# Kernel optimization log

Hardware: AMD Instinct MI355X
Metric: run time of the kernel (lower is better)

The kernel has to match this reference:

```python
import jax, jax.numpy as jnp
import numpy as np
import math

# ---- dims ----
B, N, IN_DIM = 4, 512, 128
D, H, DH = 256, 8, 32          # embed_dim, heads, dim_head
L = 8                           # performer depth
M = int(DH * math.log(DH))      # 110 FAVOR+ random features (performer_pytorch default)
HID = 256                       # lstm hidden
FF = 4 * D
EPS_K = 1e-4                    # kernel feature eps
EPS_D = 1e-6                    # denominator eps


def setup_inputs() -> dict:
    key = jax.random.key(0)
    ks = iter(jax.random.split(key, 40))
    def nrm(shape, s=0.02):
        return jax.random.normal(next(ks), shape, dtype=jnp.float32) * s
    z = lambda shape: jnp.zeros(shape, jnp.float32)
    o = lambda shape: jnp.ones(shape, jnp.float32)
    return {
        "x": jax.random.normal(next(ks), (B, N, IN_DIM), dtype=jnp.float32),
        # input projection
        "Win_w": nrm((D, IN_DIM)), "Win_b": z((D,)),
        # performer layers (stacked over L)
        "ln1_w": o((L, D)), "ln1_b": z((L, D)),
        "Wq": nrm((L, D, D)), "bq": z((L, D)),
        "Wk": nrm((L, D, D)), "bk": z((L, D)),
        "Wv": nrm((L, D, D)), "bv": z((L, D)),
        "Wo": nrm((L, D, D)), "bo": z((L, D)),
        "proj": jax.random.normal(next(ks), (L, M, DH), dtype=jnp.float32),  # FAVOR+ projections
        "ln2_w": o((L, D)), "ln2_b": z((L, D)),
        "Wff1": nrm((L, FF, D)), "bff1": z((L, FF)),
        "Wff2": nrm((L, D, FF)), "bff2": z((L, D)),
        # BiLSTM: layer0 input D, layers1-2 input 2*HID; [dir] / [layer,dir] stacks
        "Wih0": nrm((2, 4 * HID, D)), "Whh0": nrm((2, 4 * HID, HID)), "b0": z((2, 2, 4 * HID)),
        "Wih12": nrm((2, 2, 4 * HID, 2 * HID)), "Whh12": nrm((2, 2, 4 * HID, HID)), "b12": z((2, 2, 2, 4 * HID)),
        # final head
        "fc_w": nrm((1, 2 * HID)), "fc_b": z((1,)),
    }


def layer_norm(x, w, b):
    mu = jnp.mean(x, -1, keepdims=True)
    var = jnp.mean((x - mu) ** 2, -1, keepdims=True)
    return (x - mu) * jax.lax.rsqrt(var + 1e-5) * w + b


def softmax_features(x, proj, is_query):
    # FAVOR+ positive softmax-kernel features. x:[b,h,n,dh], proj:[m,dh]
    xd = x * (DH ** -0.25)
    dd = jnp.einsum('bhnd,md->bhnm', xd, proj)
    diag = 0.5 * jnp.sum(xd * xd, -1)[..., None]            # [b,h,n,1]
    if is_query:
        stab = jnp.max(dd, axis=-1, keepdims=True)
    else:
        stab = jnp.max(dd, axis=(-2, -1), keepdims=True)
    return (M ** -0.5) * (jnp.exp(dd - diag - stab) + EPS_K)


def causal_linear_attention(qp, kp, v):
    # qp,kp:[b,h,n,m], v:[b,h,n,dv] -> [b,h,n,dv]; cumulative-sum causal form
    k_cum = jnp.cumsum(kp, axis=2)
    d_inv = 1.0 / (jnp.einsum('bhnm,bhnm->bhn', qp, k_cum) + EPS_D)
    ctx = jnp.cumsum(jnp.einsum('bhnm,bhnd->bhnmd', kp, v), axis=2)
    return jnp.einsum('bhnmd,bhnm,bhn->bhnd', ctx, qp, d_inv)


def performer_block(x, p):
    (lw1, lb1, wq, bq_, wk, bk_, wv, bv_, wo, bo_, pr, lw2, lb2, w1, b1, w2, b2) = p
    b, n = x.shape[0], x.shape[1]
    y = layer_norm(x, lw1, lb1)
    sh = lambda t: t.reshape(b, n, H, DH).transpose(0, 2, 1, 3)
    q = sh(y @ wq.T + bq_)
    k = sh(y @ wk.T + bk_)
    v = sh(y @ wv.T + bv_)
    qp = softmax_features(q, pr, True)
    kp = softmax_features(k, pr, False)
    o = causal_linear_attention(qp, kp, v)
    o = o.transpose(0, 2, 1, 3).reshape(b, n, D)
    x = x + o @ wo.T + bo_
    y = layer_norm(x, lw2, lb2)
    x = x + jax.nn.gelu(y @ w1.T + b1, approximate=False) @ w2.T + b2
    return x, None


def lstm_dir(x, wih, whh, b, reverse):
    # x:[B,N,in] -> hs:[B,N,HID]; torch gate order i,f,g,o
    xs = jnp.flip(x, 1) if reverse else x
    gi = xs.transpose(1, 0, 2) @ wih.T + b                  # [N,B,4H] precomputed input part
    def step(carry, g_in):
        h, c = carry
        g = g_in + h @ whh.T
        i, f, gg, oo = jnp.split(g, 4, axis=-1)
        c = jax.nn.sigmoid(f) * c + jax.nn.sigmoid(i) * jnp.tanh(gg)
        h = jax.nn.sigmoid(oo) * jnp.tanh(c)
        return (h, c), h
    h0 = jnp.zeros((x.shape[0], HID), x.dtype)
    _, hs = jax.lax.scan(step, (h0, h0), gi)
    hs = hs.transpose(1, 0, 2)
    return jnp.flip(hs, 1) if reverse else hs


def bilstm_layer(x, wih, whh, b):
    fwd = lstm_dir(x, wih[0], whh[0], b[0, 0] + b[0, 1], False)
    bwd = lstm_dir(x, wih[1], whh[1], b[1, 0] + b[1, 1], True)
    return jnp.concatenate([fwd, bwd], -1)


def reference(x, Win_w, Win_b, ln1_w, ln1_b, Wq, bq, Wk, bk, Wv, bv, Wo, bo, proj,
              ln2_w, ln2_b, Wff1, bff1, Wff2, bff2,
              Wih0, Whh0, b0, Wih12, Whh12, b12, fc_w, fc_b):
    h = x @ Win_w.T + Win_b
    params = (ln1_w, ln1_b, Wq, bq, Wk, bk, Wv, bv, Wo, bo, proj, ln2_w, ln2_b, Wff1, bff1, Wff2, bff2)
    h, _ = jax.lax.scan(performer_block, h, params)       # 8 performer layers
    # dropout is identity at eval
    h = bilstm_layer(h, Wih0, Whh0, b0)
    h = bilstm_layer(h, Wih12[0], Whh12[0], b12[0])
    h = bilstm_layer(h, Wih12[1], Whh12[1], b12[1])
    return h[:, -1, :] @ fc_w.T + fc_b                    # [B,1]
```

## Files before the change

### kernel.cpp

```cpp
#include <hip/hip_runtime.h>
#include <math.h>

#define B_    4
#define N_    512
#define D_    256
#define H_    8
#define DH_   32
#define M_    110
#define MP_   112
#define FF_   1024
#define HID_  256
#define ROWS_ 2048
#define CHUNK 32
#define NCH   16

#define OFF_H      0u
#define OFF_Y      524288u
#define OFF_Q      1048576u
#define OFF_K      1572864u
#define OFF_V      2097152u
#define OFF_O      2621440u
#define OFF_FF     3145728u
#define OFF_QP     5242880u
#define OFF_KP     7077888u
#define OFF_S      8912896u
#define OFF_MB     9437184u
#define OFF_P      10747904u
#define OFF_KSUM   12582912u
#define OFF_PK     12640256u
#define OFF_DIAG   12697600u
#define OFF_KMAX   12713984u

#define SCALE_X 0.42044820762685725f
#define SCALE_M 0.09534625892455924f

__device__ __forceinline__ float sigmoidf_(float x){ return 1.0f/(1.0f+expf(-x)); }
__device__ __forceinline__ float geluf_(float x){ return 0.5f*x*(1.0f+erff(x*0.70710678118654752f)); }
__device__ __forceinline__ unsigned encf_(float x){ unsigned u=__float_as_uint(x); return (u&0x80000000u)?~u:(u|0x80000000u); }
__device__ __forceinline__ float decf_(unsigned u){ return (u&0x80000000u)?__uint_as_float(u&0x7fffffffu):__uint_as_float(~u); }

typedef unsigned u32x4_ __attribute__((ext_vector_type(4)));
typedef float    f32x4_ __attribute__((ext_vector_type(4)));

__device__ __forceinline__ u32x4_ ld4_l2_(const unsigned* p){
  u32x4_ v;
  asm volatile("global_load_dwordx4 %0, %1, off sc0\n\ts_waitcnt vmcnt(0)"
               : "=v"(v) : "v"(p));
  return v;
}
__device__ __forceinline__ u32x4_ ld4_far_(const unsigned* p){
  u32x4_ v;
  asm volatile("global_load_dwordx4 %0, %1, off sc0 sc1\n\ts_waitcnt vmcnt(0)"
               : "=v"(v) : "v"(p));
  return v;
}
__device__ __forceinline__ void st_l2_(float* p, float x){
  asm volatile("global_store_dword %0, %1, off sc0" :: "v"(p), "v"(x) : "memory");
}
__device__ __forceinline__ f32x4_ ld4_pin_(const float* p){
  f32x4_ v;
  asm volatile("global_load_dwordx4 %0, %1, off\n\ts_waitcnt vmcnt(0)"
               : "=v"(v) : "v"(p));
  return v;
}

__global__ __launch_bounds__(256) void gemm_k(
    const float* __restrict__ A, const float* __restrict__ W,
    const float* __restrict__ b1, const float* __restrict__ b2,
    const float* __restrict__ R, float* __restrict__ C,
    int M, int N, int K, int act)
{
  __shared__ float As[16][72];
  __shared__ float Ws[16][72];
  const int tid = threadIdx.x;
  const int tx = tid & 15, ty = tid >> 4;
  const int i0 = blockIdx.y * 64, j0 = blockIdx.x * 64;
  const int lr = tid >> 2, lc = (tid & 3) << 2;
  float acc[4][4] = {};
  for (int k0 = 0; k0 < K; k0 += 16) {
    float4 a4 = *(const float4*)(A + (size_t)(i0 + lr) * K + k0 + lc);
    float4 w4 = *(const float4*)(W + (size_t)(j0 + lr) * K + k0 + lc);
    __syncthreads();
    As[lc+0][lr]=a4.x; As[lc+1][lr]=a4.y; As[lc+2][lr]=a4.z; As[lc+3][lr]=a4.w;
    Ws[lc+0][lr]=w4.x; Ws[lc+1][lr]=w4.y; Ws[lc+2][lr]=w4.z; Ws[lc+3][lr]=w4.w;
    __syncthreads();
    #pragma unroll
    for (int kk = 0; kk < 16; kk++) {
      float4 av = *(const float4*)&As[kk][ty*4];
      float4 wv = *(const float4*)&Ws[kk][tx*4];
      acc[0][0] += av.x*wv.x; acc[0][1] += av.x*wv.y; acc[0][2] += av.x*wv.z; acc[0][3] += av.x*wv.w;
      acc[1][0] += av.y*wv.x; acc[1][1] += av.y*wv.y; acc[1][2] += av.y*wv.z; acc[1][3] += av.y*wv.w;
      acc[2][0] += av.z*wv.x; acc[2][1] += av.z*wv.y; acc[2][2] += av.z*wv.z; acc[2][3] += av.z*wv.w;
      acc[3][0] += av.w*wv.x; acc[3][1] += av.w*wv.y; acc[3][2] += av.w*wv.z; acc[3][3] += av.w*wv.w;
    }
  }
  #pragma unroll
  for (int ii = 0; ii < 4; ii++) {
    int gi_ = i0 + ty*4 + ii;
    #pragma unroll
    for (int jj = 0; jj < 4; jj++) {
      int gj = j0 + tx*4 + jj;
      float v = acc[ii][jj];
      if (b1) v += b1[gj];
      if (b2) v += b2[gj];
      if (act) v = geluf_(v);
      if (R) v += R[(size_t)gi_ * N + gj];
      C[(size_t)gi_ * N + gj] = v;
    }
  }
}

__global__ __launch_bounds__(256) void gemm3_k(
    const float* __restrict__ A,
    const float* __restrict__ W0, const float* __restrict__ W1, const float* __restrict__ W2,
    const float* __restrict__ c0_, const float* __restrict__ c1_, const float* __restrict__ c2_,
    float* __restrict__ O0, float* __restrict__ O1, float* __restrict__ O2)
{
  const int which = blockIdx.x >> 2;
  const float* W  = which == 0 ? W0 : which == 1 ? W1 : W2;
  const float* bb = which == 0 ? c0_ : which == 1 ? c1_ : c2_;
  float* C        = which == 0 ? O0 : which == 1 ? O1 : O2;
  __shared__ float As[16][72];
  __shared__ float Ws[16][72];
  const int tid = threadIdx.x;
  const int tx = tid & 15, ty = tid >> 4;
  const int i0 = blockIdx.y * 64, j0 = (blockIdx.x & 3) * 64;
  const int lr = tid >> 2, lc = (tid & 3) << 2;
  float acc[4][4] = {};
  for (int k0 = 0; k0 < 256; k0 += 16) {
    float4 a4 = *(const float4*)(A + (size_t)(i0 + lr) * 256 + k0 + lc);
    float4 w4 = *(const float4*)(W + (size_t)(j0 + lr) * 256 + k0 + lc);
    __syncthreads();
    As[lc+0][lr]=a4.x; As[lc+1][lr]=a4.y; As[lc+2][lr]=a4.z; As[lc+3][lr]=a4.w;
    Ws[lc+0][lr]=w4.x; Ws[lc+1][lr]=w4.y; Ws[lc+2][lr]=w4.z; Ws[lc+3][lr]=w4.w;
    __syncthreads();
    #pragma unroll
    for (int kk = 0; kk < 16; kk++) {
      float4 av = *(const float4*)&As[kk][ty*4];
      float4 wv = *(const float4*)&Ws[kk][tx*4];
      acc[0][0] += av.x*wv.x; acc[0][1] += av.x*wv.y; acc[0][2] += av.x*wv.z; acc[0][3] += av.x*wv.w;
      acc[1][0] += av.y*wv.x; acc[1][1] += av.y*wv.y; acc[1][2] += av.y*wv.z; acc[1][3] += av.y*wv.w;
      acc[2][0] += av.z*wv.x; acc[2][1] += av.z*wv.y; acc[2][2] += av.z*wv.z; acc[2][3] += av.z*wv.w;
      acc[3][0] += av.w*wv.x; acc[3][1] += av.w*wv.y; acc[3][2] += av.w*wv.z; acc[3][3] += av.w*wv.w;
    }
  }
  #pragma unroll
  for (int ii = 0; ii < 4; ii++) {
    int gi_ = i0 + ty*4 + ii;
    #pragma unroll
    for (int jj = 0; jj < 4; jj++) {
      int gj = j0 + tx*4 + jj;
      C[(size_t)gi_ * 256 + gj] = acc[ii][jj] + bb[gj];
    }
  }
}

__global__ __launch_bounds__(256) void gemmgi_k(
    const float* __restrict__ A, const float* __restrict__ W, const float* __restrict__ bvec,
    float* __restrict__ C, int K, int wGap, int bGap)
{
  const int dir = blockIdx.x >> 4;
  const float* Wd = W + (size_t)dir * wGap;
  const float* b1 = bvec + (size_t)dir * bGap;
  const float* b2 = b1 + 1024;
  float* Cd = C + (size_t)dir * 2097152;
  __shared__ float As[16][72];
  __shared__ float Ws[16][72];
  const int tid = threadIdx.x;
  const int tx = tid & 15, ty = tid >> 4;
  const int i0 = blockIdx.y * 64, j0 = (blockIdx.x & 15) * 64;
  const int lr = tid >> 2, lc = (tid & 3) << 2;
  float acc[4][4] = {};
  for (int k0 = 0; k0 < K; k0 += 16) {
    float4 a4 = *(const float4*)(A + (size_t)(i0 + lr) * K + k0 + lc);
    float4 w4 = *(const float4*)(Wd + (size_t)(j0 + lr) * K + k0 + lc);
    __syncthreads();
    As[lc+0][lr]=a4.x; As[lc+1][lr]=a4.y; As[lc+2][lr]=a4.z; As[lc+3][lr]=a4.w;
    Ws[lc+0][lr]=w4.x; Ws[lc+1][lr]=w4.y; Ws[lc+2][lr]=w4.z; Ws[lc+3][lr]=w4.w;
    __syncthreads();
    #pragma unroll
    for (int kk = 0; kk < 16; kk++) {
      float4 av = *(const float4*)&As[kk][ty*4];
      float4 wv = *(const float4*)&Ws[kk][tx*4];
      acc[0][0] += av.x*wv.x; acc[0][1] += av.x*wv.y; acc[0][2] += av.x*wv.z; acc[0][3] += av.x*wv.w;
      acc[1][0] += av.y*wv.x; acc[1][1] += av.y*wv.y; acc[1][2] += av.y*wv.z; acc[1][3] += av.y*wv.w;
      acc[2][0] += av.z*wv.x; acc[2][1] += av.z*wv.y; acc[2][2] += av.z*wv.z; acc[2][3] += av.z*wv.w;
      acc[3][0] += av.w*wv.x; acc[3][1] += av.w*wv.y; acc[3][2] += av.w*wv.z; acc[3][3] += av.w*wv.w;
    }
  }
  #pragma unroll
  for (int ii = 0; ii < 4; ii++) {
    int gi_ = i0 + ty*4 + ii;
    #pragma unroll
    for (int jj = 0; jj < 4; jj++) {
      int gj = j0 + tx*4 + jj;
      Cd[(size_t)gi_ * 1024 + gj] = acc[ii][jj] + b1[gj] + b2[gj];
    }
  }
}

__global__ __launch_bounds__(256) void ln_k(const float* __restrict__ x, const float* __restrict__ w,
                                            const float* __restrict__ b, float* __restrict__ y)
{
  const int row = blockIdx.x, t = threadIdx.x;
  float v = x[(size_t)row * 256 + t];
  float s = v;
  #pragma unroll
  for (int o = 32; o >= 1; o >>= 1) s += __shfl_xor(s, o, 64);
  __shared__ float w1_[4], w2_[4];
  const int wid = t >> 6, lane = t & 63;
  if (lane == 0) w1_[wid] = s;
  __syncthreads();
  float mu = (w1_[0] + w1_[1] + w1_[2] + w1_[3]) * (1.0f/256.0f);
  float d = v - mu;
  float s2 = d * d;
  #pragma unroll
  for (int o = 32; o >= 1; o >>= 1) s2 += __shfl_xor(s2, o, 64);
  if (lane == 0) w2_[wid] = s2;
  __syncthreads();
  float var = (w2_[0] + w2_[1] + w2_[2] + w2_[3]) * (1.0f/256.0f);
  y[(size_t)row * 256 + t] = d * (1.0f / sqrtf(var + 1e-5f)) * w[t] + b[t];
}

__global__ __launch_bounds__(256) void feat_k(const float* __restrict__ q, const float* __restrict__ kk,
                                              const float* __restrict__ proj,
                                              float* __restrict__ qp, float* __restrict__ kpraw,
                                              float* __restrict__ diagb, unsigned* __restrict__ kmax)
{
  const int isq = (blockIdx.x < 4096);
  const int bx = isq ? blockIdx.x : (blockIdx.x - 4096);
  const int wid = threadIdx.x >> 6, lane = threadIdx.x & 63;
  const int p = bx * 4 + wid;
  const int bh = p >> 9, n = p & 511;
  const int b = bh >> 3, h = bh & 7;
  __shared__ float xs[4][32];
  const float* xrow = (isq ? q : kk) + ((size_t)(b * N_ + n)) * D_ + h * DH_;
  if (lane < 32) xs[wid][lane] = xrow[lane] * SCALE_X;
  __syncthreads();
  float diag = 0.f;
  #pragma unroll
  for (int d = 0; d < 32; d++) { float xv = xs[wid][d]; diag += xv * xv; }
  diag *= 0.5f;
  const int m0 = lane, m1 = 64 + lane;
  float dd0 = 0.f, dd1 = -INFINITY;
  #pragma unroll
  for (int d = 0; d < 32; d++) dd0 += xs[wid][d] * proj[m0 * 32 + d];
  if (m1 < M_) {
    float a = 0.f;
    #pragma unroll
    for (int d = 0; d < 32; d++) a += xs[wid][d] * proj[m1 * 32 + d];
    dd1 = a;
  }
  float mx = fmaxf(dd0, dd1);
  #pragma unroll
  for (int o = 32; o >= 1; o >>= 1) mx = fmaxf(mx, __shfl_xor(mx, o, 64));
  if (isq) {
    float* out = qp + (size_t)p * MP_;
    out[m0] = SCALE_M * (expf(dd0 - diag - mx) + 1e-4f);
    if (m1 < M_)        out[m1] = SCALE_M * (expf(dd1 - diag - mx) + 1e-4f);
    else if (m1 < MP_)  out[m1] = 0.f;
  } else {
    float* out = kpraw + (size_t)p * MP_;
    out[m0] = dd0;
    if (m1 < M_) out[m1] = dd1;
    if (lane == 0) { diagb[p] = diag; atomicMax(kmax + bh, encf_(mx)); }
  }
}

__global__ __launch_bounds__(256) void csum_k(const float* __restrict__ kp, const float* __restrict__ v,
                                              const float* __restrict__ diagb, const unsigned* __restrict__ kmax,
                                              float* __restrict__ S, float* __restrict__ ksum)
{
  const int bh = blockIdx.x >> 4, c = blockIdx.x & 15;
  const int b = bh >> 3, h = bh & 7;
  __shared__ float kpc[CHUNK * MP_];
  __shared__ float vc[CHUNK][DH_];
  const float* kpbase = kp + ((size_t)bh * N_ + c * CHUNK) * MP_;
  const float kmx = decf_(kmax[bh]);
  const int r0 = bh * N_ + c * CHUNK;
  for (int f = threadIdx.x; f < CHUNK * MP_; f += 256) {
    int i = f / MP_, m = f - i * MP_;
    float raw = kpbase[f];
    float val = 0.f;
    if (m < M_) val = SCALE_M * (expf(raw - diagb[r0 + i] - kmx) + 1e-4f);
    kpc[f] = val;
  }
  for (int f = threadIdx.x; f < CHUNK * DH_; f += 256) {
    int i = f >> 5, d = f & 31;
    vc[i][d] = v[((size_t)(b * N_ + c * CHUNK + i)) * D_ + h * DH_ + d];
  }
  __syncthreads();
  const int d = threadIdx.x & 31, mg = threadIdx.x >> 5;
  float Sa[14] = {};
  for (int i = 0; i < CHUNK; i++) {
    float vv = vc[i][d];
    #pragma unroll
    for (int j = 0; j < 14; j++) Sa[j] += kpc[i * MP_ + mg * 14 + j] * vv;
  }
  float* Sout = S + (((size_t)blockIdx.x) * MP_ + mg * 14) * DH_ + d;
  #pragma unroll
  for (int j = 0; j < 14; j++) Sout[(size_t)j * DH_] = Sa[j];
  if (threadIdx.x < MP_) {
    float s = 0.f;
    for (int i = 0; i < CHUNK; i++) s += kpc[i * MP_ + threadIdx.x];
    ksum[(size_t)blockIdx.x * MP_ + threadIdx.x] = s;
  }
}

__global__ __launch_bounds__(256) void cpref_k(const float* __restrict__ S, const float* __restrict__ ksum,
                                               float* __restrict__ P, float* __restrict__ pk)
{
  const int bh = blockIdx.x;
  const int d = threadIdx.x & 31, mg = threadIdx.x >> 5;
  float run[14] = {};
  for (int c = 0; c < NCH; c++) {
    size_t base = (((size_t)(bh * NCH + c)) * MP_ + mg * 14) * DH_ + d;
    #pragma unroll
    for (int j = 0; j < 14; j++) { P[base + (size_t)j * DH_] = run[j]; run[j] += S[base + (size_t)j * DH_]; }
  }
  if (threadIdx.x < MP_) {
    float r = 0.f;
    for (int c = 0; c < NCH; c++) {
      size_t o = (size_t)(bh * NCH + c) * MP_ + threadIdx.x;
      pk[o] = r; r += ksum[o];
    }
  }
}

__global__ __launch_bounds__(256, 1) void attn_k(const float* __restrict__ qp, const float* __restrict__ kp,
                                                 const float* __restrict__ v, const float* __restrict__ P,
                                                 const float* __restrict__ pk,
                                                 const float* __restrict__ diagb, const unsigned* __restrict__ kmax,
                                                 float* __restrict__ o)
{
  const int bh = blockIdx.x >> 4, c = blockIdx.x & 15;
  const int b = bh >> 3, h = bh & 7;
  __shared__ float qpc[CHUNK * 113];
  __shared__ float kpc[CHUNK * 113];
  __shared__ float vc[CHUNK][DH_];
  __shared__ float Pl[MP_ * DH_];
  __shared__ float pkl[MP_];
  __shared__ float Al[CHUNK * 33];
  __shared__ float den[CHUNK];
  const int t = threadIdx.x;
  const float* qbase = qp + ((size_t)bh * N_ + c * CHUNK) * MP_;
  const float* kbase = kp + ((size_t)bh * N_ + c * CHUNK) * MP_;
  const float kmx = decf_(kmax[bh]);
  const int r0 = bh * N_ + c * CHUNK;
  for (int f = t; f < CHUNK * MP_; f += 256) {
    int i = f / MP_, m = f - i * MP_;
    qpc[i * 113 + m] = qbase[f];
    float raw = kbase[f];
    float val = 0.f;
    if (m < M_) val = SCALE_M * (expf(raw - diagb[r0 + i] - kmx) + 1e-4f);
    kpc[i * 113 + m] = val;
  }
  for (int f = t; f < CHUNK * DH_; f += 256) {
    int i = f >> 5, d = f & 31;
    vc[i][d] = v[((size_t)(b * N_ + c * CHUNK + i)) * D_ + h * DH_ + d];
  }
  for (int f = t; f < MP_ * DH_; f += 256) Pl[f] = P[((size_t)blockIdx.x) * MP_ * DH_ + f];
  if (t < MP_) pkl[t] = pk[(size_t)blockIdx.x * MP_ + t];
  __syncthreads();
  {
    const int ti = t >> 4, tj = t & 15;
    float a00 = 0.f, a01 = 0.f, a10 = 0.f, a11 = 0.f;
    for (int m = 0; m < MP_; m++) {
      float q0 = qpc[(ti*2+0)*113 + m], q1 = qpc[(ti*2+1)*113 + m];
      float k0 = kpc[(tj*2+0)*113 + m], k1 = kpc[(tj*2+1)*113 + m];
      a00 += q0*k0; a01 += q0*k1; a10 += q1*k0; a11 += q1*k1;
    }
    const int i0_ = ti*2, j0_ = tj*2;
    Al[(i0_  )*33 + j0_  ] = (j0_   <= i0_  ) ? a00 : 0.f;
    Al[(i0_  )*33 + j0_+1] = (j0_+1 <= i0_  ) ? a01 : 0.f;
    Al[(i0_+1)*33 + j0_  ] = (j0_   <= i0_+1) ? a10 : 0.f;
    Al[(i0_+1)*33 + j0_+1] = (j0_+1 <= i0_+1) ? a11 : 0.f;
  }
  __syncthreads();
  if (t < CHUNK) {
    const int i = t; float s = 0.f;
    for (int m = 0; m < MP_; m++) s += qpc[i*113 + m] * pkl[m];
    for (int j = 0; j <= i; j++) s += Al[i*33 + j];
    den[i] = 1.0f / (s + 1e-6f);
  }
  __syncthreads();
  {
    const int d = t & 31, ig = t >> 5;
    float Pd[MP_];
    #pragma unroll
    for (int m = 0; m < MP_; m++) Pd[m] = Pl[m * DH_ + d];
    float vd[CHUNK];
    #pragma unroll
    for (int j = 0; j < CHUNK; j++) vd[j] = vc[j][d];
    for (int r = 0; r < 4; r++) {
      const int i = ig * 4 + r;
      float acc = 0.f;
      #pragma unroll
      for (int m = 0; m < MP_; m++) acc += qpc[i*113 + m] * Pd[m];
      #pragma unroll
      for (int j = 0; j < CHUNK; j++) acc += Al[i*33 + j] * vd[j];
      o[((size_t)(b * N_ + c * CHUNK + i)) * D_ + h * DH_ + d] = acc * den[i];
    }
  }
}

__global__ __launch_bounds__(256, 1) void rec_k(
    const float* __restrict__ gi, const float* __restrict__ whh,
    float* __restrict__ hs, float* __restrict__ hxa, float* __restrict__ hxb)
{
  const int bid = blockIdx.x;
  if ((bid & 7) > 1) return;
  const int dir = bid & 7;
  const int s = bid >> 3;
  if (s >= 16) return;
  const int t = threadIdx.x;

  const float* giD = gi + (size_t)dir * 2097152;
  const float* whD = whh + (size_t)dir * 262144;
  float* hxaD = hxa + (size_t)dir * 524288;
  float* hxbD = hxb + (size_t)dir * 524288;

  __shared__ __align__(16) float h_sh[4][256];
  __shared__ __align__(16) float red[64 * 33];

  __builtin_amdgcn_fence(__ATOMIC_ACQUIRE, "agent");

  const int rg = t & 31, kq = t >> 5;
  f32x4_ w4[2][8];
  #pragma unroll
  for (int rr = 0; rr < 2; rr++) {
    const int rho = rg * 2 + rr;
    const int grow = (rho >> 4) * 256 + s * 16 + (rho & 15);
    const float* src = whD + (size_t)grow * 256 + kq * 32;
    #pragma unroll
    for (int q = 0; q < 8; q++) w4[rr][q] = ld4_pin_(src + q * 4);
  }

  const int j = t & 15, bb = t >> 4;
  const float* pgi0 = giD + (size_t)bb * 524288 + (size_t)(s * 16 + j);

  ((float4*)h_sh)[t] = make_float4(0.f, 0.f, 0.f, 0.f);
  float c0 = 0.f;
  __syncthreads();

  int n = dir ? 511 : 0;
  float gnext[4];
  if (t < 64) {
    #pragma unroll
    for (int g = 0; g < 4; g++) gnext[g] = pgi0[(size_t)n * 1024 + g * 256];
  }

  for (int step = 0; step < 512; step++) {
    const int n2 = dir ? (510 - step) : (step + 1);
    float gcur[4];
    if (t < 64) {
      #pragma unroll
      for (int g = 0; g < 4; g++) gcur[g] = gnext[g];
      if (step < 511) {
        #pragma unroll
        for (int g = 0; g < 4; g++) gnext[g] = pgi0[(size_t)n2 * 1024 + g * 256];
      }
    }

    float acc[2][4] = {};
    #pragma unroll
    for (int q = 0; q < 8; q++) {
      f32x4_ h0 = *(const f32x4_*)&h_sh[0][kq * 32 + q * 4];
      f32x4_ h1 = *(const f32x4_*)&h_sh[1][kq * 32 + q * 4];
      f32x4_ h2 = *(const f32x4_*)&h_sh[2][kq * 32 + q * 4];
      f32x4_ h3 = *(const f32x4_*)&h_sh[3][kq * 32 + q * 4];
      #pragma unroll
      for (int rr = 0; rr < 2; rr++) {
        f32x4_ w = w4[rr][q];
        acc[rr][0] += w.x*h0.x + w.y*h0.y + w.z*h0.z + w.w*h0.w;
        acc[rr][1] += w.x*h1.x + w.y*h1.y + w.z*h1.z + w.w*h1.w;
        acc[rr][2] += w.x*h2.x + w.y*h2.y + w.z*h2.z + w.w*h2.w;
        acc[rr][3] += w.x*h3.x + w.y*h3.y + w.z*h3.z + w.w*h3.w;
      }
    }
    #pragma unroll
    for (int rr = 0; rr < 2; rr++)
      #pragma unroll
      for (int b = 0; b < 4; b++)
        red[(rg * 2 + rr) * 33 + b * 8 + kq] = acc[rr][b];
    __syncthreads();

    if (t < 64) {
      float pre[4];
      #pragma unroll
      for (int g = 0; g < 4; g++) {
        const float* rp = &red[(g * 16 + j) * 33 + bb * 8];
        float sum = gcur[g];
        #pragma unroll
        for (int q = 0; q < 8; q++) sum += rp[q];
        pre[g] = sum;
      }
      c0 = sigmoidf_(pre[1]) * c0 + sigmoidf_(pre[0]) * tanhf(pre[2]);
      const float hv = sigmoidf_(pre[3]) * tanhf(c0);
      hs[(size_t)(bb * 512 + n) * 512 + dir * 256 + s * 16 + j] = hv;
      if (step < 511) {
        const size_t off = (size_t)step * 1024 + bb * 256 + s * 16 + j;
        st_l2_(hxaD + off, hv);
        __hip_atomic_store(hxbD + off, hv, __ATOMIC_RELAXED,
                           __HIP_MEMORY_SCOPE_AGENT);
      }
    }

    if (step < 511) {
      const unsigned* pa = (const unsigned*)(hxaD + (size_t)step * 1024) + t * 4;
      const unsigned* pb = (const unsigned*)(hxbD + (size_t)step * 1024) + t * 4;
      u32x4_ v = ld4_l2_(pa);
      int it = 0;
      while (v.x == 0xFFFFFFFFu || v.y == 0xFFFFFFFFu ||
             v.z == 0xFFFFFFFFu || v.w == 0xFFFFFFFFu) {
        ++it;
        v = ((it & 3) == 3) ? ld4_far_(pb) : ld4_l2_(pa);
      }
      float4 hv4;
      hv4.x = __uint_as_float(v.x); hv4.y = __uint_as_float(v.y);
      hv4.z = __uint_as_float(v.z); hv4.w = __uint_as_float(v.w);
      ((float4*)h_sh)[t] = hv4;
      __syncthreads();
    }
    n = n2;
  }
}

__global__ __launch_bounds__(256) void fc_k(const float* __restrict__ hs, const float* __restrict__ fw,
                                            const float* __restrict__ fb, float* __restrict__ out)
{
  const int t = threadIdx.x;
  float p[4] = {};
  for (int j = t; j < 512; j += 256) {
    const float w = fw[j];
    #pragma unroll
    for (int b = 0; b < 4; b++) p[b] += hs[(size_t)(b * 512 + 511) * 512 + j] * w;
  }
  #pragma unroll
  for (int b = 0; b < 4; b++)
    #pragma unroll
    for (int o = 32; o >= 1; o >>= 1) p[b] += __shfl_xor(p[b], o, 64);
  __shared__ float r4[4][4];
  const int wid = t >> 6, lane = t & 63;
  if (lane == 0) {
    #pragma unroll
    for (int b = 0; b < 4; b++) r4[b][wid] = p[b];
  }
  __syncthreads();
  if (t == 0) {
    #pragma unroll
    for (int b = 0; b < 4; b++) out[b] = r4[b][0] + r4[b][1] + r4[b][2] + r4[b][3] + fb[0];
  }
}

extern "C" void kernel_launch(void* const* d_in, const int* in_sizes, int n_in,
                              void* d_out, int out_size, void* d_ws, size_t ws_size,
                              hipStream_t stream) {
  (void)in_sizes; (void)n_in; (void)out_size; (void)ws_size;
  const float* x     = (const float*)d_in[0];
  const float* Win_w = (const float*)d_in[1];
  const float* Win_b = (const float*)d_in[2];
  const float* ln1w  = (const float*)d_in[3];
  const float* ln1b  = (const float*)d_in[4];
  const float* Wq    = (const float*)d_in[5];
  const float* bq    = (const float*)d_in[6];
  const float* Wk    = (const float*)d_in[7];
  const float* bk    = (const float*)d_in[8];
  const float* Wv    = (const float*)d_in[9];
  const float* bv    = (const float*)d_in[10];
  const float* Wo    = (const float*)d_in[11];
  const float* bo    = (const float*)d_in[12];
  const float* proj  = (const float*)d_in[13];
  const float* ln2w  = (const float*)d_in[14];
  const float* ln2b  = (const float*)d_in[15];
  const float* Wff1  = (const float*)d_in[16];
  const float* bff1  = (const float*)d_in[17];
  const float* Wff2  = (const float*)d_in[18];
  const float* bff2  = (const float*)d_in[19];
  const float* Wih0  = (const float*)d_in[20];
  const float* Whh0  = (const float*)d_in[21];
  const float* b0    = (const float*)d_in[22];
  const float* Wih12 = (const float*)d_in[23];
  const float* Whh12 = (const float*)d_in[24];
  const float* b12   = (const float*)d_in[25];
  const float* fcw   = (const float*)d_in[26];
  const float* fcb   = (const float*)d_in[27];

  float* ws = (float*)d_ws;
  float* H   = ws + OFF_H;
  float* Y   = ws + OFF_Y;
  float* Q   = ws + OFF_Q;
  float* Kb  = ws + OFF_K;
  float* V   = ws + OFF_V;
  float* O   = ws + OFF_O;
  float* FFb = ws + OFF_FF;
  float* QP  = ws + OFF_QP;
  float* KP  = ws + OFF_KP;
  float* S   = ws + OFF_S;
  float* P   = ws + OFF_P;
  float* KS  = ws + OFF_KSUM;
  float* PK  = ws + OFF_PK;
  float* DG  = ws + OFF_DIAG;
  unsigned* KMAX = (unsigned*)(ws + OFF_KMAX);
  float* GI  = ws + OFF_QP;
  float* MA  = ws + OFF_MB;
  float* MB0 = ws + OFF_Y;
  float* MB1 = ws + OFF_K;
  float* BLa = ws + OFF_FF;
  float* BLb = ws + OFF_FF + 1048576;

  const dim3 blk(256);
  const dim3 g256(4, 32);
  const dim3 g768(12, 32);
  const dim3 g1024(16, 32);
  const dim3 g2048(32, 32);

  gemm_k<<<g256, blk, 0, stream>>>(x, Win_w, Win_b, nullptr, nullptr, H, ROWS_, 256, 128, 0);

  for (int l = 0; l < 8; l++) {
    const float* prj = proj + (size_t)l * 3520;
    ln_k<<<ROWS_, blk, 0, stream>>>(H, ln1w + l*256, ln1b + l*256, Y);
    gemm3_k<<<g768, blk, 0, stream>>>(Y, Wq + (size_t)l*65536, Wk + (size_t)l*65536, Wv + (size_t)l*65536,
                                      bq + l*256, bk + l*256, bv + l*256, Q, Kb, V);
    (void)hipMemsetAsync(KMAX, 0, 32 * sizeof(unsigned), stream);
    feat_k<<<8192, blk, 0, stream>>>(Q, Kb, prj, QP, KP, DG, KMAX);
    csum_k<<<512, blk, 0, stream>>>(KP, V, DG, KMAX, S, KS);
    cpref_k<<<32, blk, 0, stream>>>(S, KS, P, PK);
    attn_k<<<512, blk, 0, stream>>>(QP, KP, V, P, PK, DG, KMAX, O);
    gemm_k<<<g256, blk, 0, stream>>>(O, Wo + (size_t)l*65536, bo + l*256, nullptr, H, H, ROWS_, 256, 256, 0);
    ln_k<<<ROWS_, blk, 0, stream>>>(H, ln2w + l*256, ln2b + l*256, Y);
    gemm_k<<<g1024, blk, 0, stream>>>(Y, Wff1 + (size_t)l*262144, bff1 + l*1024, nullptr, nullptr, FFb, ROWS_, 1024, 256, 1);
    gemm_k<<<g256, blk, 0, stream>>>(FFb, Wff2 + (size_t)l*262144, bff2 + l*256, nullptr, H, H, ROWS_, 256, 1024, 0);
  }

  (void)hipMemsetAsync(MA, 0xFF, 3145728u * sizeof(float), stream);
  (void)hipMemsetAsync(MB0, 0xFF, 2097152u * sizeof(float), stream);

  gemmgi_k<<<g2048, blk, 0, stream>>>(H, Wih0, b0, GI, 256, 262144, 2048);
  rec_k<<<128, blk, 0, stream>>>(GI, Whh0, BLa, MA, MB0);
  (void)hipMemsetAsync(MB0, 0xFF, 1048576u * sizeof(float), stream);

  gemmgi_k<<<g2048, blk, 0, stream>>>(BLa, Wih12, b12, GI, 512, 524288, 2048);
  rec_k<<<128, blk, 0, stream>>>(GI, Whh12, BLb, MA + 1048576, MB1);

  gemmgi_k<<<g2048, blk, 0, stream>>>(BLb, Wih12 + 1048576, b12 + 4096, GI, 512, 524288, 2048);
  rec_k<<<128, blk, 0, stream>>>(GI, Whh12 + 524288, BLa, MA + 2097152, MB0);

  fc_k<<<1, blk, 0, stream>>>(BLa, fcw, fcb, (float*)d_out);
}
```

Measured before the change: 7.346 ms.

## Claim LSTM recurrence slots per XCC and stage recurrent weights in LDS

The recurrent kernel now picks its direction and slot at runtime: each block reads its XCC id and takes a slot from a per-direction atomic counter, so all blocks of one direction sit on the same XCC and their cross-block exchange of hidden state stays in a shared L2. Blocks on other XCCs wait and then claim any slots left over. The recurrent weight slice moves from pinned registers into a large dynamic LDS buffer, which frees registers but adds LDS reads on every timestep. The change also adds a counter memset before each launch and depends on how the hardware places blocks, so placement is not deterministic.

Result: slower. 13.72 ms (+86.8%).

```diff
diff --git a/kernel.cpp b/kernel.cpp
--- a/kernel.cpp
+++ b/kernel.cpp
@@ -30,9 +30,16 @@
 #define OFF_PK     12640256u
 #define OFF_DIAG   12697600u
 #define OFF_KMAX   12713984u
+#define OFF_CLM    12714048u
 
 #define SCALE_X 0.42044820762685725f
 #define SCALE_M 0.09534625892455924f
+
+#define REC_WLDS   0
+#define REC_HSH    16640
+#define REC_RED    17664
+#define REC_LDSF   19776
+#define REC_LDSB   79104
 
 __device__ __forceinline__ float sigmoidf_(float x){ return 1.0f/(1.0f+expf(-x)); }
 __device__ __forceinline__ float geluf_(float x){ return 0.5f*x*(1.0f+erff(x*0.70710678118654752f)); }
@@ -56,12 +63,6 @@
 }
 __device__ __forceinline__ void st_l2_(float* p, float x){
   asm volatile("global_store_dword %0, %1, off sc0" :: "v"(p), "v"(x) : "memory");
-}
-__device__ __forceinline__ f32x4_ ld4_pin_(const float* p){
-  f32x4_ v;
-  asm volatile("global_load_dwordx4 %0, %1, off\n\ts_waitcnt vmcnt(0)"
-               : "=v"(v) : "v"(p));
-  return v;
 }
 
 __global__ __launch_bounds__(256) void gemm_k(
@@ -406,40 +407,70 @@
 
 __global__ __launch_bounds__(256, 1) void rec_k(
     const float* __restrict__ gi, const float* __restrict__ whh,
-    float* __restrict__ hs, float* __restrict__ hxa, float* __restrict__ hxb)
-{
-  const int bid = blockIdx.x;
-  if ((bid & 7) > 1) return;
-  const int dir = bid & 7;
-  const int s = bid >> 3;
-  if (s >= 16) return;
+    float* __restrict__ hs, float* __restrict__ hxa, float* __restrict__ hxb,
+    unsigned* __restrict__ claim)
+{
+  extern __shared__ float dynlds[];
+  float* wlds  = dynlds + REC_WLDS;
+  float* h_shf = dynlds + REC_HSH;
+  float* redf  = dynlds + REC_RED;
+  __shared__ int sel[2];
+
   const int t = threadIdx.x;
+
+  __builtin_amdgcn_fence(__ATOMIC_ACQUIRE, "agent");
+
+  if (t == 0) {
+    unsigned xcc;
+    asm volatile("s_getreg_b32 %0, hwreg(HW_REG_XCC_ID)" : "=s"(xcc));
+    xcc &= 7u;
+    int slot = -1, dir = -1;
+    if (xcc < 2u) {
+      unsigned s0 = atomicAdd(&claim[xcc], 1u);
+      if (s0 < 16u) { slot = (int)s0; dir = (int)xcc; }
+    }
+    if (slot < 0) {
+      for (int w = 0; w < 96; ++w) {
+        unsigned c0 = __hip_atomic_load(&claim[0], __ATOMIC_RELAXED, __HIP_MEMORY_SCOPE_AGENT);
+        unsigned c1 = __hip_atomic_load(&claim[1], __ATOMIC_RELAXED, __HIP_MEMORY_SCOPE_AGENT);
+        if (c0 >= 16u && c1 >= 16u) break;
+        __builtin_amdgcn_s_sleep(15);
+      }
+      for (int d = 0; d < 2 && slot < 0; ++d) {
+        unsigned c = __hip_atomic_load(&claim[d], __ATOMIC_RELAXED, __HIP_MEMORY_SCOPE_AGENT);
+        if (c < 16u) {
+          unsigned s0 = atomicAdd(&claim[d], 1u);
+          if (s0 < 16u) { slot = (int)s0; dir = d; }
+        }
+      }
+    }
+    sel[0] = slot; sel[1] = dir;
+  }
+  __syncthreads();
+  const int s = sel[0], dir = sel[1];
+  if (s < 0) return;
 
   const float* giD = gi + (size_t)dir * 2097152;
   const float* whD = whh + (size_t)dir * 262144;
   float* hxaD = hxa + (size_t)dir * 524288;
   float* hxbD = hxb + (size_t)dir * 524288;
 
-  __shared__ __align__(16) float h_sh[4][256];
-  __shared__ __align__(16) float red[64 * 33];
-
-  __builtin_amdgcn_fence(__ATOMIC_ACQUIRE, "agent");
-
   const int rg = t & 31, kq = t >> 5;
-  f32x4_ w4[2][8];
+
   #pragma unroll
   for (int rr = 0; rr < 2; rr++) {
-    const int rho = rg * 2 + rr;
+    const int rho = rg + 32 * rr;
     const int grow = (rho >> 4) * 256 + s * 16 + (rho & 15);
-    const float* src = whD + (size_t)grow * 256 + kq * 32;
-    #pragma unroll
-    for (int q = 0; q < 8; q++) w4[rr][q] = ld4_pin_(src + q * 4);
+    const float* srcw = whD + (size_t)grow * 256 + kq * 32;
+    float* dstw = wlds + rho * 260 + kq * 32;
+    #pragma unroll
+    for (int q = 0; q < 8; q++) *(float4*)(dstw + q * 4) = *(const float4*)(srcw + q * 4);
   }
 
   const int j = t & 15, bb = t >> 4;
   const float* pgi0 = giD + (size_t)bb * 524288 + (size_t)(s * 16 + j);
 
-  ((float4*)h_sh)[t] = make_float4(0.f, 0.f, 0.f, 0.f);
+  ((float4*)h_shf)[t] = make_float4(0.f, 0.f, 0.f, 0.f);
   float c0 = 0.f;
   __syncthreads();
 
@@ -465,13 +496,13 @@
     float acc[2][4] = {};
     #pragma unroll
     for (int q = 0; q < 8; q++) {
-      f32x4_ h0 = *(const f32x4_*)&h_sh[0][kq * 32 + q * 4];
-      f32x4_ h1 = *(const f32x4_*)&h_sh[1][kq * 32 + q * 4];
-      f32x4_ h2 = *(const f32x4_*)&h_sh[2][kq * 32 + q * 4];
-      f32x4_ h3 = *(const f32x4_*)&h_sh[3][kq * 32 + q * 4];
+      f32x4_ h0 = *(const f32x4_*)&h_shf[0 * 256 + kq * 32 + q * 4];
+      f32x4_ h1 = *(const f32x4_*)&h_shf[1 * 256 + kq * 32 + q * 4];
+      f32x4_ h2 = *(const f32x4_*)&h_shf[2 * 256 + kq * 32 + q * 4];
+      f32x4_ h3 = *(const f32x4_*)&h_shf[3 * 256 + kq * 32 + q * 4];
       #pragma unroll
       for (int rr = 0; rr < 2; rr++) {
-        f32x4_ w = w4[rr][q];
+        f32x4_ w = *(const f32x4_*)&wlds[(rg + 32 * rr) * 260 + kq * 32 + q * 4];
         acc[rr][0] += w.x*h0.x + w.y*h0.y + w.z*h0.z + w.w*h0.w;
         acc[rr][1] += w.x*h1.x + w.y*h1.y + w.z*h1.z + w.w*h1.w;
         acc[rr][2] += w.x*h2.x + w.y*h2.y + w.z*h2.z + w.w*h2.w;
@@ -482,14 +513,14 @@
     for (int rr = 0; rr < 2; rr++)
       #pragma unroll
       for (int b = 0; b < 4; b++)
-        red[(rg * 2 + rr) * 33 + b * 8 + kq] = acc[rr][b];
+        redf[(rg + 32 * rr) * 33 + b * 8 + kq] = acc[rr][b];
     __syncthreads();
 
     if (t < 64) {
       float pre[4];
       #pragma unroll
       for (int g = 0; g < 4; g++) {
-        const float* rp = &red[(g * 16 + j) * 33 + bb * 8];
+        const float* rp = &redf[(g * 16 + j) * 33 + bb * 8];
         float sum = gcur[g];
         #pragma unroll
         for (int q = 0; q < 8; q++) sum += rp[q];
@@ -519,7 +550,7 @@
       float4 hv4;
       hv4.x = __uint_as_float(v.x); hv4.y = __uint_as_float(v.y);
       hv4.z = __uint_as_float(v.z); hv4.w = __uint_as_float(v.w);
-      ((float4*)h_sh)[t] = hv4;
+      ((float4*)h_shf)[t] = hv4;
       __syncthreads();
     }
     n = n2;
@@ -602,12 +633,20 @@
   float* PK  = ws + OFF_PK;
   float* DG  = ws + OFF_DIAG;
   unsigned* KMAX = (unsigned*)(ws + OFF_KMAX);
+  unsigned* CLM  = (unsigned*)(ws + OFF_CLM);
   float* GI  = ws + OFF_QP;
   float* MA  = ws + OFF_MB;
   float* MB0 = ws + OFF_Y;
   float* MB1 = ws + OFF_K;
   float* BLa = ws + OFF_FF;
   float* BLb = ws + OFF_FF + 1048576;
+
+  static bool attr_set = false;
+  if (!attr_set) {
+    (void)hipFuncSetAttribute(reinterpret_cast<const void*>(rec_k),
+                              hipFuncAttributeMaxDynamicSharedMemorySize, REC_LDSB);
+    attr_set = true;
+  }
 
   const dim3 blk(256);
   const dim3 g256(4, 32);
@@ -637,14 +676,17 @@
   (void)hipMemsetAsync(MB0, 0xFF, 2097152u * sizeof(float), stream);
 
   gemmgi_k<<<g2048, blk, 0, stream>>>(H, Wih0, b0, GI, 256, 262144, 2048);
-  rec_k<<<128, blk, 0, stream>>>(GI, Whh0, BLa, MA, MB0);
+  (void)hipMemsetAsync(CLM, 0, 64, stream);
+  rec_k<<<128, blk, REC_LDSB, stream>>>(GI, Whh0, BLa, MA, MB0, CLM);
   (void)hipMemsetAsync(MB0, 0xFF, 1048576u * sizeof(float), stream);
 
   gemmgi_k<<<g2048, blk, 0, stream>>>(BLa, Wih12, b12, GI, 512, 524288, 2048);
-  rec_k<<<128, blk, 0, stream>>>(GI, Whh12, BLb, MA + 1048576, MB1);
+  (void)hipMemsetAsync(CLM, 0, 64, stream);
+  rec_k<<<128, blk, REC_LDSB, stream>>>(GI, Whh12, BLb, MA + 1048576, MB1, CLM);
 
   gemmgi_k<<<g2048, blk, 0, stream>>>(BLb, Wih12 + 1048576, b12 + 4096, GI, 512, 524288, 2048);
-  rec_k<<<128, blk, 0, stream>>>(GI, Whh12 + 524288, BLa, MA + 2097152, MB0);
+  (void)hipMemsetAsync(CLM, 0, 64, stream);
+  rec_k<<<128, blk, REC_LDSB, stream>>>(GI, Whh12 + 524288, BLa, MA + 2097152, MB0, CLM);
 
   fc_k<<<1, blk, 0, stream>>>(BLa, fcw, fcb, (float*)d_out);
 }
```
